# Optimization experiments

Measured on AMD Instinct MI355X. Metric: run time of the kernel, lower is better.

The kernel has to match this reference:

```python
import jax, jax.numpy as jnp
import numpy as np

EMBED_DIM = 1024
HEADS = 16
D_K = EMBED_DIM // HEADS
B, S = 2, 2048


def setup_inputs() -> dict:
    key = jax.random.key(0)
    ks = jax.random.split(key, 8)
    scale = 1.0 / np.sqrt(EMBED_DIM)
    inp = {
        "key": jax.random.normal(ks[0], (B, S, EMBED_DIM), dtype=jnp.float32),
        "query": jax.random.normal(ks[1], (B, S, EMBED_DIM), dtype=jnp.float32),
        "value": jax.random.normal(ks[2], (B, S, EMBED_DIM), dtype=jnp.float32),
        # torch nn.Linear stores weight as [out, in]; y = x @ W.T
        "Wq": jax.random.normal(ks[3], (EMBED_DIM, EMBED_DIM), dtype=jnp.float32) * scale,
        "Wk": jax.random.normal(ks[4], (EMBED_DIM, EMBED_DIM), dtype=jnp.float32) * scale,
        "Wv": jax.random.normal(ks[5], (EMBED_DIM, EMBED_DIM), dtype=jnp.float32) * scale,
        "Wo": jax.random.normal(ks[6], (EMBED_DIM, EMBED_DIM), dtype=jnp.float32) * scale,
        "bo": jax.random.normal(ks[7], (EMBED_DIM,), dtype=jnp.float32) * scale,
        # causal mask, True = keep (matches masked_fill(~mask, -1e20))
        "mask": jnp.tril(jnp.ones((S, S), dtype=jnp.bool_))[None, None, :, :],
    }
    return inp


def _split_heads(x):
    b, s, _ = x.shape
    return x.reshape(b, s, HEADS, D_K).transpose(0, 2, 1, 3)  # [B,H,S,d_k]


def reference(key, query, value, Wq, Wk, Wv, Wo, bo, mask):
    b, q_len = query.shape[0], query.shape[1]
    k = _split_heads(key @ Wk.T)
    q = _split_heads(query @ Wq.T)
    v = _split_heads(value @ Wv.T)
    scores = jnp.einsum('bhqd,bhkd->bhqk', q, k) / np.sqrt(D_K)
    scores = jnp.where(mask, scores, jnp.float32(-1e20))
    attn = jax.nn.softmax(scores, axis=-1)
    out = jnp.einsum('bhqk,bhkd->bhqd', attn, v)
    out = out.transpose(0, 2, 1, 3).reshape(b, q_len, HEADS * D_K)
    return out @ Wo.T + bo
```

## Files before the change

### kernel.cpp

```cpp
#include <hip/hip_runtime.h>
#include <cstdint>
#include <cstddef>


typedef __bf16 bf16;
typedef __bf16 bf16x4 __attribute__((ext_vector_type(4)));
typedef __bf16 bf16x8 __attribute__((ext_vector_type(8)));
typedef float f32x4 __attribute__((ext_vector_type(4)));

#define MFMA(a, b, c) __builtin_amdgcn_mfma_f32_16x16x32_bf16(a, b, c, 0, 0, 0)

constexpr int EMBED = 1024;
constexpr int SEQ = 2048;
constexpr int HEADS = 16;
constexpr int DK = 64;
constexpr int BH = 32;

__device__ __forceinline__ void gl16(const bf16* g, bf16* l) {
  __builtin_amdgcn_global_load_lds(
      (const __attribute__((address_space(1))) unsigned int*)g,
      (__attribute__((address_space(3))) unsigned int*)l, 16, 0, 0);
}

struct ConvArgs {
  const void* src[8];
  bf16* dst[8];
  int n8[8];
  const unsigned short* probe;
};

__global__ __launch_bounds__(256) void convert_kernel(ConvArgs a) {
  __shared__ int cnt;
  const int t = threadIdx.x;
  if (t == 0) cnt = 0;
  __syncthreads();
  {
    unsigned short u = a.probe[2 * t];
    int e = (u >> 7) & 0xFF;
    if (e >= 100 && e <= 130) atomicAdd(&cnt, 1);
  }
  __syncthreads();
  const int isf32 = (cnt < 128) ? 1 : 0;

  const int seg = blockIdx.y;
  const void* s = a.src[seg];
  bf16* d = a.dst[seg];
  const int n8 = a.n8[seg];
  for (int i = blockIdx.x * 256 + t; i < n8; i += gridDim.x * 256) {
    if (isf32) {
      const float* sp = (const float*)s + (size_t)i * 8;
      float4 x = *(const float4*)sp, y = *(const float4*)(sp + 4);
      bf16x8 v;
      v[0] = (bf16)x.x; v[1] = (bf16)x.y; v[2] = (bf16)x.z; v[3] = (bf16)x.w;
      v[4] = (bf16)y.x; v[5] = (bf16)y.y; v[6] = (bf16)y.z; v[7] = (bf16)y.w;
      *(bf16x8*)(d + (size_t)i * 8) = v;
    } else {
      *(uint4*)(d + (size_t)i * 8) = *(const uint4*)((const bf16*)s + (size_t)i * 8);
    }
  }
}

__device__ __forceinline__ void gemm_body(
    const bf16* __restrict__ X, const bf16* __restrict__ W,
    const bf16* __restrict__ bias, bf16* __restrict__ outb,
    float* __restrict__ outf, int mode, bf16* As, bf16* Bs, int m0, int n0)
{
  const int t = threadIdx.x;
  const int lane = t & 63, wave = t >> 6;
  const int wm = wave >> 2, wn = wave & 3;
  const int l16 = lane & 15, quad = lane >> 4;

  f32x4 acc[4][2] = {};

  for (int k0 = 0; k0 < EMBED; k0 += 64) {
    __syncthreads();
#pragma unroll
    for (int i = 0; i < 2; ++i) {
      int idx = t + i * 512;
      int r = idx >> 3;
      int cl = (idx & 7) ^ (r & 7);
      gl16(X + (size_t)(m0 + r) * EMBED + k0 + cl * 8, As + (i * 512 + wave * 64) * 8);
      gl16(W + (size_t)(n0 + r) * EMBED + k0 + cl * 8, Bs + (i * 512 + wave * 64) * 8);
    }
    __syncthreads();

#pragma unroll
    for (int ks = 0; ks < 2; ++ks) {
      bf16x8 a[4], b[2];
#pragma unroll
      for (int mi = 0; mi < 4; ++mi) {
        int row = wm * 64 + mi * 16 + l16;
        a[mi] = *(const bf16x8*)(As + row * 64 + (((ks * 4 + quad) ^ (row & 7)) * 8));
      }
#pragma unroll
      for (int ni = 0; ni < 2; ++ni) {
        int row = wn * 32 + ni * 16 + l16;
        b[ni] = *(const bf16x8*)(Bs + row * 64 + (((ks * 4 + quad) ^ (row & 7)) * 8));
      }
#pragma unroll
      for (int mi = 0; mi < 4; ++mi)
#pragma unroll
        for (int ni = 0; ni < 2; ++ni)
          acc[mi][ni] = MFMA(a[mi], b[ni], acc[mi][ni]);
    }
  }

#pragma unroll
  for (int mi = 0; mi < 4; ++mi) {
#pragma unroll
    for (int ni = 0; ni < 2; ++ni) {
      int n = n0 + wn * 32 + ni * 16 + l16;
#pragma unroll
      for (int r = 0; r < 4; ++r) {
        int m = m0 + wm * 64 + mi * 16 + quad * 4 + r;
        float v = acc[mi][ni][r];
        if (mode == 2) {
          outf[(size_t)m * EMBED + n] = v + (float)bias[n];
        } else {
          int b_ = m >> 11, s = m & (SEQ - 1);
          int h = n >> 6, d = n & 63;
          int bh = b_ * HEADS + h;
          if (mode == 0)
            outb[((size_t)bh * SEQ + s) * DK + d] = (bf16)v;
          else
            outb[((size_t)bh * DK + d) * SEQ + s] = (bf16)v;
        }
      }
    }
  }
}

struct QkvArgs {
  const bf16 *X0, *X1, *X2;
  const bf16 *W0, *W1, *W2;
  bf16 *O0, *O1, *O2;
};

__global__ __launch_bounds__(512, 4) void qkv_gemm(QkvArgs args) {
  __shared__ alignas(16) bf16 As[128 * 64];
  __shared__ alignas(16) bf16 Bs[128 * 64];
  const int z = blockIdx.z;
  const bf16* X = (z == 0) ? args.X0 : (z == 1) ? args.X1 : args.X2;
  const bf16* W = (z == 0) ? args.W0 : (z == 1) ? args.W1 : args.W2;
  bf16* O      = (z == 0) ? args.O0 : (z == 1) ? args.O1 : args.O2;
  int mode = (z == 2) ? 1 : 0;
  gemm_body(X, W, nullptr, O, nullptr, mode, As, Bs,
            blockIdx.x * 128, blockIdx.y * 128);
}

__global__ __launch_bounds__(512, 4) void out_gemm(const bf16* __restrict__ X,
                                                   const bf16* __restrict__ W,
                                                   const bf16* __restrict__ bias,
                                                   float* __restrict__ out) {
  __shared__ alignas(16) bf16 As[128 * 64];
  __shared__ alignas(16) bf16 Bs[128 * 64];
  gemm_body(X, W, bias, nullptr, out, 2, As, Bs,
            blockIdx.x * 128, blockIdx.y * 128);
}

__global__ __launch_bounds__(256, 6) void attn_kernel(
    const bf16* __restrict__ qbuf, const bf16* __restrict__ kbuf,
    const bf16* __restrict__ vtbuf, bf16* __restrict__ ctx)
{
  __shared__ alignas(16) bf16 Ks[64 * 64];
  __shared__ alignas(16) bf16 VTs[64 * 64];
  __shared__ alignas(16) bf16 Ps[64 * 72];

  const int t = threadIdx.x;
  const int g = (blockIdx.x + blockIdx.y) & 31;
  const int qt = (blockIdx.y & 16) ? (31 - g) : g;
  const int bh = blockIdx.y;
  const int q0 = qt * 64;
  const int lane = t & 63, w = t >> 6;
  const int l16 = lane & 15, quad = lane >> 4;

  const bf16* Kp0 = kbuf + (size_t)bh * SEQ * DK;
  const bf16* Vp0 = vtbuf + (size_t)bh * DK * SEQ;

  const bf16* Qg = qbuf + ((size_t)bh * SEQ + q0 + w * 16 + l16) * DK;
  bf16x8 qf[2];
  qf[0] = *(const bf16x8*)(Qg + quad * 8);
  qf[1] = *(const bf16x8*)(Qg + 32 + quad * 8);

  const int qglob = q0 + w * 16 + l16;
  float lst = 0.f;
  f32x4 o[4] = {};
  bf16* Pw = Ps + w * 16 * 72;

  constexpr float SC = 0.125f * 1.44269504f;
  constexpr float BI = -8.0f * 1.44269504f;

#pragma unroll 1
  for (int kt = 0; kt < qt; ++kt) {
    __syncthreads();
    const bf16* Kg = Kp0 + (size_t)kt * 64 * DK;
    const bf16* Vg = Vp0 + (size_t)kt * 64;
#pragma unroll
    for (int i = 0; i < 2; ++i) {
      int idx = t + i * 256;
      int r = idx >> 3;
      int cl = (idx & 7) ^ (r & 7);
      gl16(Kg + (size_t)r * DK + cl * 8, Ks + (i * 256 + w * 64) * 8);
      gl16(Vg + (size_t)r * SEQ + cl * 8, VTs + (i * 256 + w * 64) * 8);
    }
    __syncthreads();

    f32x4 sacc[4] = {};
#pragma unroll
    for (int ks = 0; ks < 2; ++ks) {
#pragma unroll
      for (int mi = 0; mi < 4; ++mi) {
        int row = mi * 16 + l16;
        bf16x8 kf = *(const bf16x8*)(Ks + row * 64 + (((ks * 4 + quad) ^ (row & 7)) * 8));
        sacc[mi] = MFMA(kf, qf[ks], sacc[mi]);
      }
    }

    float ls = 0.f;
#pragma unroll
    for (int mi = 0; mi < 4; ++mi) {
      bf16x4 pv;
#pragma unroll
      for (int r = 0; r < 4; ++r) {
        float p = __builtin_exp2f(__builtin_fmaf(sacc[mi][r], SC, BI));
        ls += p;
        pv[r] = (bf16)p;
      }
      *(bf16x4*)(Pw + l16 * 72 + mi * 16 + quad * 4) = pv;
    }
    ls += __shfl_xor(ls, 16);
    ls += __shfl_xor(ls, 32);
    lst += ls;

    __builtin_amdgcn_s_setprio(1);
#pragma unroll
    for (int ks = 0; ks < 2; ++ks) {
      bf16x8 pf = *(const bf16x8*)(Pw + l16 * 72 + ks * 32 + quad * 8);
#pragma unroll
      for (int dt = 0; dt < 4; ++dt) {
        int row = dt * 16 + l16;
        bf16x8 vf = *(const bf16x8*)(VTs + row * 64 +
                                     (((ks * 4 + quad) ^ (row & 7)) * 8));
        o[dt] = MFMA(vf, pf, o[dt]);
      }
    }
    __builtin_amdgcn_s_setprio(0);
  }

  {
    const int kt = qt;
    __syncthreads();
    const bf16* Kg = Kp0 + (size_t)kt * 64 * DK;
    const bf16* Vg = Vp0 + (size_t)kt * 64;
#pragma unroll
    for (int i = 0; i < 2; ++i) {
      int idx = t + i * 256;
      int r = idx >> 3;
      int cl = (idx & 7) ^ (r & 7);
      gl16(Kg + (size_t)r * DK + cl * 8, Ks + (i * 256 + w * 64) * 8);
      gl16(Vg + (size_t)r * SEQ + cl * 8, VTs + (i * 256 + w * 64) * 8);
    }
    __syncthreads();

    f32x4 sacc[4] = {};
#pragma unroll
    for (int ks = 0; ks < 2; ++ks) {
#pragma unroll
      for (int mi = 0; mi < 4; ++mi) {
        int row = mi * 16 + l16;
        bf16x8 kf = *(const bf16x8*)(Ks + row * 64 + (((ks * 4 + quad) ^ (row & 7)) * 8));
        sacc[mi] = MFMA(kf, qf[ks], sacc[mi]);
      }
    }

    float ls = 0.f;
    const int kbase = kt * 64 + quad * 4;
#pragma unroll
    for (int mi = 0; mi < 4; ++mi) {
      bf16x4 pv;
#pragma unroll
      for (int r = 0; r < 4; ++r) {
        float arg = __builtin_fmaf(sacc[mi][r], SC, BI);
        if (kbase + mi * 16 + r > qglob) arg = -1e30f;
        float p = __builtin_exp2f(arg);
        ls += p;
        pv[r] = (bf16)p;
      }
      *(bf16x4*)(Pw + l16 * 72 + mi * 16 + quad * 4) = pv;
    }
    ls += __shfl_xor(ls, 16);
    ls += __shfl_xor(ls, 32);
    lst += ls;

    __builtin_amdgcn_s_setprio(1);
#pragma unroll
    for (int ks = 0; ks < 2; ++ks) {
      bf16x8 pf = *(const bf16x8*)(Pw + l16 * 72 + ks * 32 + quad * 8);
#pragma unroll
      for (int dt = 0; dt < 4; ++dt) {
        int row = dt * 16 + l16;
        bf16x8 vf = *(const bf16x8*)(VTs + row * 64 +
                                     (((ks * 4 + quad) ^ (row & 7)) * 8));
        o[dt] = MFMA(vf, pf, o[dt]);
      }
    }
    __builtin_amdgcn_s_setprio(0);
  }

  const float inv = 1.0f / lst;
  const int b_ = bh >> 4, h = bh & 15;
  bf16* dst = ctx + ((size_t)b_ * SEQ + qglob) * EMBED + h * DK;
#pragma unroll
  for (int dt = 0; dt < 4; ++dt) {
    bf16x4 v;
#pragma unroll
    for (int r = 0; r < 4; ++r) v[r] = (bf16)(o[dt][r] * inv);
    *(bf16x4*)(dst + dt * 16 + quad * 4) = v;
  }
}

extern "C" void kernel_launch(void* const* d_in, const int* in_sizes, int n_in,
                              void* d_out, int out_size, void* d_ws, size_t ws_size,
                              hipStream_t stream) {
  const void* key   = d_in[0];
  const void* query = d_in[1];
  const void* value = d_in[2];
  const void* Wq    = d_in[3];
  const void* Wk    = d_in[4];
  const void* Wv    = d_in[5];
  const void* Wo    = d_in[6];
  const void* bo    = d_in[7];
  float* out = (float*)d_out;

  char* base = (char*)d_ws + 256;
  const size_t XN = (size_t)2 * SEQ * EMBED;
  const size_t WN = (size_t)EMBED * EMBED;
  const size_t per = (size_t)BH * SEQ * DK;

  bf16* cq  = (bf16*)base;
  bf16* ck  = cq + XN;
  bf16* cv  = ck + XN;
  bf16* cWq = cv + XN;
  bf16* cWk = cWq + WN;
  bf16* cWv = cWk + WN;
  bf16* cWo = cWv + WN;
  bf16* cbo = cWo + WN;
  bf16* qb  = cbo + 1024;
  bf16* kb  = qb + per;
  bf16* vtb = kb + per;
  bf16* ctx = vtb + per;

  ConvArgs ca;
  ca.src[0] = query; ca.dst[0] = cq;  ca.n8[0] = (int)(XN / 8);
  ca.src[1] = key;   ca.dst[1] = ck;  ca.n8[1] = (int)(XN / 8);
  ca.src[2] = value; ca.dst[2] = cv;  ca.n8[2] = (int)(XN / 8);
  ca.src[3] = Wq;    ca.dst[3] = cWq; ca.n8[3] = (int)(WN / 8);
  ca.src[4] = Wk;    ca.dst[4] = cWk; ca.n8[4] = (int)(WN / 8);
  ca.src[5] = Wv;    ca.dst[5] = cWv; ca.n8[5] = (int)(WN / 8);
  ca.src[6] = Wo;    ca.dst[6] = cWo; ca.n8[6] = (int)(WN / 8);
  ca.src[7] = bo;    ca.dst[7] = cbo; ca.n8[7] = 128;
  ca.probe = (const unsigned short*)Wq;
  convert_kernel<<<dim3(512, 8), 256, 0, stream>>>(ca);

  QkvArgs qa{cq, ck, cv, cWq, cWk, cWv, qb, kb, vtb};
  qkv_gemm<<<dim3(32, 8, 3), 512, 0, stream>>>(qa);
  attn_kernel<<<dim3(32, 32), 256, 0, stream>>>(qb, kb, vtb, ctx);
  out_gemm<<<dim3(32, 8), 512, 0, stream>>>(ctx, cWo, cbo, out);
}
```

Baseline: 229.0 us.

## Split attention key tiles across two wave halves with LDS reduction

The attention kernel now launches 512 threads per block instead of 256. Two groups of four waves each handle one 32-key half of every 64-key tile for the same 16 query rows. Their partial output accumulators and row sums are combined through shared memory at the end. This doubles the waves per block, which should add latency hiding and cut the serial per-wave work in long causal rows. The cost is an extra cross-wave reduction and more waves sharing the same barriers.

```diff
diff --git a/kernel.cpp b/kernel.cpp
--- a/kernel.cpp
+++ b/kernel.cpp
@@ -158,13 +158,77 @@
             blockIdx.x * 128, blockIdx.y * 128);
 }
 
-__global__ __launch_bounds__(256, 6) void attn_kernel(
+template<bool MASKED>
+__device__ __forceinline__ void attn_step(
+    int kt, int t, int w, int half, int l16, int quad, int qglob,
+    const bf16* __restrict__ Kp0, const bf16* __restrict__ Vp0,
+    bf16* Ks, bf16* VTs, bf16* Pw,
+    const bf16x8 qf[2], f32x4 o[4], float& lst)
+{
+  constexpr float SC = 0.125f * 1.44269504f;
+  constexpr float BI = -8.0f * 1.44269504f;
+
+  __syncthreads();
+  {
+    int r = t >> 3;
+    int cl = (t & 7) ^ (r & 7);
+    gl16(Kp0 + ((size_t)kt * 64 + r) * DK + cl * 8, Ks + w * 512);
+    gl16(Vp0 + (size_t)r * SEQ + kt * 64 + cl * 8, VTs + w * 512);
+  }
+  __syncthreads();
+
+  f32x4 sacc[2] = {};
+#pragma unroll
+  for (int ks = 0; ks < 2; ++ks) {
+#pragma unroll
+    for (int mi = 0; mi < 2; ++mi) {
+      int row = half * 32 + mi * 16 + l16;
+      bf16x8 kf = *(const bf16x8*)(Ks + row * 64 + (((ks * 4 + quad) ^ (row & 7)) * 8));
+      sacc[mi] = MFMA(kf, qf[ks], sacc[mi]);
+    }
+  }
+
+  float ls = 0.f;
+#pragma unroll
+  for (int mi = 0; mi < 2; ++mi) {
+    bf16x4 pv;
+#pragma unroll
+    for (int r = 0; r < 4; ++r) {
+      float arg = __builtin_fmaf(sacc[mi][r], SC, BI);
+      if (MASKED) {
+        int kg = kt * 64 + half * 32 + mi * 16 + quad * 4 + r;
+        if (kg > qglob) arg = -1e30f;
+      }
+      float p = __builtin_exp2f(arg);
+      ls += p;
+      pv[r] = (bf16)p;
+    }
+    *(bf16x4*)(Pw + l16 * 36 + mi * 16 + quad * 4) = pv;
+  }
+  ls += __shfl_xor(ls, 16);
+  ls += __shfl_xor(ls, 32);
+  lst += ls;
+
+  __builtin_amdgcn_s_setprio(1);
+  bf16x8 pf = *(const bf16x8*)(Pw + l16 * 36 + quad * 8);
+#pragma unroll
+  for (int dt = 0; dt < 4; ++dt) {
+    int row = dt * 16 + l16;
+    bf16x8 vf = *(const bf16x8*)(VTs + row * 64 +
+                                 (((half * 4 + quad) ^ (row & 7)) * 8));
+    o[dt] = MFMA(vf, pf, o[dt]);
+  }
+  __builtin_amdgcn_s_setprio(0);
+}
+
+__global__ __launch_bounds__(512, 8) void attn_kernel(
     const bf16* __restrict__ qbuf, const bf16* __restrict__ kbuf,
     const bf16* __restrict__ vtbuf, bf16* __restrict__ ctx)
 {
-  __shared__ alignas(16) bf16 Ks[64 * 64];
-  __shared__ alignas(16) bf16 VTs[64 * 64];
-  __shared__ alignas(16) bf16 Ps[64 * 72];
+  __shared__ alignas(16) unsigned char SM[25600];
+  bf16* Ks  = (bf16*)SM;
+  bf16* VTs = (bf16*)(SM + 8192);
+  bf16* Ps  = (bf16*)(SM + 16384);
 
   const int t = threadIdx.x;
   const int g = (blockIdx.x + blockIdx.y) & 31;
@@ -172,150 +236,53 @@
   const int bh = blockIdx.y;
   const int q0 = qt * 64;
   const int lane = t & 63, w = t >> 6;
+  const int wq = w & 3, half = w >> 2;
   const int l16 = lane & 15, quad = lane >> 4;
 
   const bf16* Kp0 = kbuf + (size_t)bh * SEQ * DK;
   const bf16* Vp0 = vtbuf + (size_t)bh * DK * SEQ;
 
-  const bf16* Qg = qbuf + ((size_t)bh * SEQ + q0 + w * 16 + l16) * DK;
+  const bf16* Qg = qbuf + ((size_t)bh * SEQ + q0 + wq * 16 + l16) * DK;
   bf16x8 qf[2];
   qf[0] = *(const bf16x8*)(Qg + quad * 8);
   qf[1] = *(const bf16x8*)(Qg + 32 + quad * 8);
 
-  const int qglob = q0 + w * 16 + l16;
+  const int qglob = q0 + wq * 16 + l16;
   float lst = 0.f;
   f32x4 o[4] = {};
-  bf16* Pw = Ps + w * 16 * 72;
-
-  constexpr float SC = 0.125f * 1.44269504f;
-  constexpr float BI = -8.0f * 1.44269504f;
+  bf16* Pw = Ps + w * (16 * 36);
 
 #pragma unroll 1
-  for (int kt = 0; kt < qt; ++kt) {
-    __syncthreads();
-    const bf16* Kg = Kp0 + (size_t)kt * 64 * DK;
-    const bf16* Vg = Vp0 + (size_t)kt * 64;
-#pragma unroll
-    for (int i = 0; i < 2; ++i) {
-      int idx = t + i * 256;
-      int r = idx >> 3;
-      int cl = (idx & 7) ^ (r & 7);
-      gl16(Kg + (size_t)r * DK + cl * 8, Ks + (i * 256 + w * 64) * 8);
-      gl16(Vg + (size_t)r * SEQ + cl * 8, VTs + (i * 256 + w * 64) * 8);
-    }
-    __syncthreads();
-
-    f32x4 sacc[4] = {};
-#pragma unroll
-    for (int ks = 0; ks < 2; ++ks) {
-#pragma unroll
-      for (int mi = 0; mi < 4; ++mi) {
-        int row = mi * 16 + l16;
-        bf16x8 kf = *(const bf16x8*)(Ks + row * 64 + (((ks * 4 + quad) ^ (row & 7)) * 8));
-        sacc[mi] = MFMA(kf, qf[ks], sacc[mi]);
-      }
-    }
-
-    float ls = 0.f;
-#pragma unroll
-    for (int mi = 0; mi < 4; ++mi) {
-      bf16x4 pv;
-#pragma unroll
-      for (int r = 0; r < 4; ++r) {
-        float p = __builtin_exp2f(__builtin_fmaf(sacc[mi][r], SC, BI));
-        ls += p;
-        pv[r] = (bf16)p;
-      }
-      *(bf16x4*)(Pw + l16 * 72 + mi * 16 + quad * 4) = pv;
-    }
-    ls += __shfl_xor(ls, 16);
-    ls += __shfl_xor(ls, 32);
-    lst += ls;
-
-    __builtin_amdgcn_s_setprio(1);
-#pragma unroll
-    for (int ks = 0; ks < 2; ++ks) {
-      bf16x8 pf = *(const bf16x8*)(Pw + l16 * 72 + ks * 32 + quad * 8);
-#pragma unroll
-      for (int dt = 0; dt < 4; ++dt) {
-        int row = dt * 16 + l16;
-        bf16x8 vf = *(const bf16x8*)(VTs + row * 64 +
-                                     (((ks * 4 + quad) ^ (row & 7)) * 8));
-        o[dt] = MFMA(vf, pf, o[dt]);
-      }
-    }
-    __builtin_amdgcn_s_setprio(0);
-  }
-
-  {
-    const int kt = qt;
-    __syncthreads();
-    const bf16* Kg = Kp0 + (size_t)kt * 64 * DK;
-    const bf16* Vg = Vp0 + (size_t)kt * 64;
-#pragma unroll
-    for (int i = 0; i < 2; ++i) {
-      int idx = t + i * 256;
-      int r = idx >> 3;
-      int cl = (idx & 7) ^ (r & 7);
-      gl16(Kg + (size_t)r * DK + cl * 8, Ks + (i * 256 + w * 64) * 8);
-      gl16(Vg + (size_t)r * SEQ + cl * 8, VTs + (i * 256 + w * 64) * 8);
-    }
-    __syncthreads();
-
-    f32x4 sacc[4] = {};
-#pragma unroll
-    for (int ks = 0; ks < 2; ++ks) {
-#pragma unroll
-      for (int mi = 0; mi < 4; ++mi) {
-        int row = mi * 16 + l16;
-        bf16x8 kf = *(const bf16x8*)(Ks + row * 64 + (((ks * 4 + quad) ^ (row & 7)) * 8));
-        sacc[mi] = MFMA(kf, qf[ks], sacc[mi]);
-      }
-    }
-
-    float ls = 0.f;
-    const int kbase = kt * 64 + quad * 4;
-#pragma unroll
-    for (int mi = 0; mi < 4; ++mi) {
-      bf16x4 pv;
-#pragma unroll
-      for (int r = 0; r < 4; ++r) {
-        float arg = __builtin_fmaf(sacc[mi][r], SC, BI);
-        if (kbase + mi * 16 + r > qglob) arg = -1e30f;
-        float p = __builtin_exp2f(arg);
-        ls += p;
-        pv[r] = (bf16)p;
-      }
-      *(bf16x4*)(Pw + l16 * 72 + mi * 16 + quad * 4) = pv;
-    }
-    ls += __shfl_xor(ls, 16);
-    ls += __shfl_xor(ls, 32);
-    lst += ls;
-
-    __builtin_amdgcn_s_setprio(1);
-#pragma unroll
-    for (int ks = 0; ks < 2; ++ks) {
-      bf16x8 pf = *(const bf16x8*)(Pw + l16 * 72 + ks * 32 + quad * 8);
-#pragma unroll
-      for (int dt = 0; dt < 4; ++dt) {
-        int row = dt * 16 + l16;
-        bf16x8 vf = *(const bf16x8*)(VTs + row * 64 +
-                                     (((ks * 4 + quad) ^ (row & 7)) * 8));
-        o[dt] = MFMA(vf, pf, o[dt]);
-      }
-    }
-    __builtin_amdgcn_s_setprio(0);
-  }
-
-  const float inv = 1.0f / lst;
-  const int b_ = bh >> 4, h = bh & 15;
-  bf16* dst = ctx + ((size_t)b_ * SEQ + qglob) * EMBED + h * DK;
-#pragma unroll
-  for (int dt = 0; dt < 4; ++dt) {
-    bf16x4 v;
-#pragma unroll
-    for (int r = 0; r < 4; ++r) v[r] = (bf16)(o[dt][r] * inv);
-    *(bf16x4*)(dst + dt * 16 + quad * 4) = v;
+  for (int kt = 0; kt < qt; ++kt)
+    attn_step<false>(kt, t, w, half, l16, quad, qglob, Kp0, Vp0, Ks, VTs, Pw, qf, o, lst);
+  attn_step<true>(qt, t, w, half, l16, quad, qglob, Kp0, Vp0, Ks, VTs, Pw, qf, o, lst);
+
+  __syncthreads();
+  float* Co = (float*)SM;
+  float* Cl = (float*)(SM + 16384);
+  if (half) {
+    int base = ((w - 4) * 64 + lane) * 16;
+#pragma unroll
+    for (int dt = 0; dt < 4; ++dt) *(f32x4*)(Co + base + dt * 4) = o[dt];
+    Cl[(w - 4) * 64 + lane] = lst;
+  }
+  __syncthreads();
+  if (!half) {
+    int base = (w * 64 + lane) * 16;
+#pragma unroll
+    for (int dt = 0; dt < 4; ++dt) o[dt] += *(const f32x4*)(Co + base + dt * 4);
+    lst += Cl[w * 64 + lane];
+
+    const float inv = 1.0f / lst;
+    const int b_ = bh >> 4, h = bh & 15;
+    bf16* dst = ctx + ((size_t)b_ * SEQ + qglob) * EMBED + h * DK;
+#pragma unroll
+    for (int dt = 0; dt < 4; ++dt) {
+      bf16x4 v;
+#pragma unroll
+      for (int r = 0; r < 4; ++r) v[r] = (bf16)(o[dt][r] * inv);
+      *(bf16x4*)(dst + dt * 16 + quad * 4) = v;
+    }
   }
 }
 
@@ -364,6 +331,6 @@
 
   QkvArgs qa{cq, ck, cv, cWq, cWk, cWv, qb, kb, vtb};
   qkv_gemm<<<dim3(32, 8, 3), 512, 0, stream>>>(qa);
-  attn_kernel<<<dim3(32, 32), 256, 0, stream>>>(qb, kb, vtb, ctx);
+  attn_kernel<<<dim3(32, 32), 512, 0, stream>>>(qb, kb, vtb, ctx);
   out_gemm<<<dim3(32, 8), 512, 0, stream>>>(ctx, cWo, cbo, out);
 }
```

New measurement: 247.5 us. +8.1%, slower.

## Split long causal attention rows across two blocks with a combine kernel

Applied to the files above, without the earlier changes.

Causal attention for query tiles 16-31 is split into two blocks, one covering KV tiles 0-15 and one covering the rest. Each writes unnormalized fp32 partial outputs and row sums to workspace, and a new combine kernel merges them into ctx. The aim is to even out per-block work and cut the tail caused by the longest query tiles. The cost is an extra kernel launch, fp32 partial traffic, and a workspace-size check that falls back to the monolithic kernel when space is short. The combine is valid because a fixed exponent bias is used instead of a running max.

```diff
diff --git a/kernel.cpp b/kernel.cpp
--- a/kernel.cpp
+++ b/kernel.cpp
@@ -158,7 +158,166 @@
             blockIdx.x * 128, blockIdx.y * 128);
 }
 
-__global__ __launch_bounds__(256, 6) void attn_kernel(
+template<bool MASKED>
+__device__ __forceinline__ void attn_tile(
+    int kt, int t, int w, int l16, int quad, int qglob,
+    const bf16* __restrict__ Kp0, const bf16* __restrict__ Vp0,
+    bf16* Ks, bf16* VTs, bf16* Pw,
+    const bf16x8 qf[2], f32x4 o[4], float& lst)
+{
+  constexpr float SC = 0.125f * 1.44269504f;
+  constexpr float BI = -8.0f * 1.44269504f;
+
+  __syncthreads();
+  const bf16* Kg = Kp0 + (size_t)kt * 64 * DK;
+  const bf16* Vg = Vp0 + (size_t)kt * 64;
+#pragma unroll
+  for (int i = 0; i < 2; ++i) {
+    int idx = t + i * 256;
+    int r = idx >> 3;
+    int cl = (idx & 7) ^ (r & 7);
+    gl16(Kg + (size_t)r * DK + cl * 8, Ks + (i * 256 + w * 64) * 8);
+    gl16(Vg + (size_t)r * SEQ + cl * 8, VTs + (i * 256 + w * 64) * 8);
+  }
+  __syncthreads();
+
+  f32x4 sacc[4] = {};
+#pragma unroll
+  for (int ks = 0; ks < 2; ++ks) {
+#pragma unroll
+    for (int mi = 0; mi < 4; ++mi) {
+      int row = mi * 16 + l16;
+      bf16x8 kf = *(const bf16x8*)(Ks + row * 64 + (((ks * 4 + quad) ^ (row & 7)) * 8));
+      sacc[mi] = MFMA(kf, qf[ks], sacc[mi]);
+    }
+  }
+
+  float ls = 0.f;
+  const int kbase = kt * 64 + quad * 4;
+#pragma unroll
+  for (int mi = 0; mi < 4; ++mi) {
+    bf16x4 pv;
+#pragma unroll
+    for (int r = 0; r < 4; ++r) {
+      float arg = __builtin_fmaf(sacc[mi][r], SC, BI);
+      if (MASKED && (kbase + mi * 16 + r > qglob)) arg = -1e30f;
+      float p = __builtin_exp2f(arg);
+      ls += p;
+      pv[r] = (bf16)p;
+    }
+    *(bf16x4*)(Pw + l16 * 72 + mi * 16 + quad * 4) = pv;
+  }
+  ls += __shfl_xor(ls, 16);
+  ls += __shfl_xor(ls, 32);
+  lst += ls;
+
+  __builtin_amdgcn_s_setprio(1);
+#pragma unroll
+  for (int ks = 0; ks < 2; ++ks) {
+    bf16x8 pf = *(const bf16x8*)(Pw + l16 * 72 + ks * 32 + quad * 8);
+#pragma unroll
+    for (int dt = 0; dt < 4; ++dt) {
+      int row = dt * 16 + l16;
+      bf16x8 vf = *(const bf16x8*)(VTs + row * 64 +
+                                   (((ks * 4 + quad) ^ (row & 7)) * 8));
+      o[dt] = MFMA(vf, pf, o[dt]);
+    }
+  }
+  __builtin_amdgcn_s_setprio(0);
+}
+
+__global__ __launch_bounds__(256, 6) void attn_split(
+    const bf16* __restrict__ qbuf, const bf16* __restrict__ kbuf,
+    const bf16* __restrict__ vtbuf, bf16* __restrict__ ctx,
+    float* __restrict__ po, float* __restrict__ pl)
+{
+  __shared__ alignas(16) bf16 Ks[64 * 64];
+  __shared__ alignas(16) bf16 VTs[64 * 64];
+  __shared__ alignas(16) bf16 Ps[64 * 72];
+
+  const int t = threadIdx.x;
+  const int s = blockIdx.x;
+  const int bh = blockIdx.y;
+  const int mode = (s < 16) ? 0 : (s < 32) ? 1 : 2;
+  const int qt = (mode == 2) ? (s - 16) : s;
+  const int t0 = (mode == 2) ? 16 : 0;
+  const int t1 = (mode == 1) ? 15 : qt;
+  const int q0 = qt * 64;
+  const int lane = t & 63, w = t >> 6;
+  const int l16 = lane & 15, quad = lane >> 4;
+
+  const bf16* Kp0 = kbuf + (size_t)bh * SEQ * DK;
+  const bf16* Vp0 = vtbuf + (size_t)bh * DK * SEQ;
+
+  const bf16* Qg = qbuf + ((size_t)bh * SEQ + q0 + w * 16 + l16) * DK;
+  bf16x8 qf[2];
+  qf[0] = *(const bf16x8*)(Qg + quad * 8);
+  qf[1] = *(const bf16x8*)(Qg + 32 + quad * 8);
+
+  const int qglob = q0 + w * 16 + l16;
+  float lst = 0.f;
+  f32x4 o[4] = {};
+  bf16* Pw = Ps + w * 16 * 72;
+
+  const int tEnd = (mode == 1) ? t1 : t1 - 1;
+#pragma unroll 1
+  for (int kt = t0; kt <= tEnd; ++kt)
+    attn_tile<false>(kt, t, w, l16, quad, qglob, Kp0, Vp0, Ks, VTs, Pw, qf, o, lst);
+  if (mode != 1)
+    attn_tile<true>(t1, t, w, l16, quad, qglob, Kp0, Vp0, Ks, VTs, Pw, qf, o, lst);
+
+  if (mode == 0) {
+    const float inv = 1.0f / lst;
+    const int b_ = bh >> 4, h = bh & 15;
+    bf16* dst = ctx + ((size_t)b_ * SEQ + qglob) * EMBED + h * DK;
+#pragma unroll
+    for (int dt = 0; dt < 4; ++dt) {
+      bf16x4 v;
+#pragma unroll
+      for (int r = 0; r < 4; ++r) v[r] = (bf16)(o[dt][r] * inv);
+      *(bf16x4*)(dst + dt * 16 + quad * 4) = v;
+    }
+  } else {
+    const int p = ((bh << 4) + (qt - 16)) * 2 + (mode - 1);
+    float* ob = po + (size_t)p * 4096;
+    const int qloc = w * 16 + l16;
+#pragma unroll
+    for (int dt = 0; dt < 4; ++dt)
+      *(f32x4*)(ob + qloc * 64 + dt * 16 + quad * 4) = o[dt];
+    if (quad == 0) pl[(size_t)p * 64 + qloc] = lst;
+  }
+}
+
+__global__ __launch_bounds__(256) void attn_combine(
+    const float* __restrict__ po, const float* __restrict__ pl,
+    bf16* __restrict__ ctx)
+{
+  const int p0 = blockIdx.x;
+  const int bh = p0 >> 4, qtl = p0 & 15, qt = 16 + qtl;
+  const int t = threadIdx.x;
+  const float* o0 = po + (size_t)p0 * 2 * 4096;
+  const float* o1 = o0 + 4096;
+  const float* l0 = pl + (size_t)p0 * 2 * 64;
+  const float* l1 = l0 + 64;
+
+  const int q = t >> 2;
+  const int d0 = (t & 3) * 16;
+  const float inv = 1.0f / (l0[q] + l1[q]);
+
+  const int b_ = bh >> 4, h = bh & 15;
+  bf16* dst = ctx + ((size_t)b_ * SEQ + qt * 64 + q) * EMBED + h * DK + d0;
+#pragma unroll
+  for (int j = 0; j < 4; ++j) {
+    f32x4 a = *(const f32x4*)(o0 + q * 64 + d0 + j * 4);
+    f32x4 b = *(const f32x4*)(o1 + q * 64 + d0 + j * 4);
+    bf16x4 v;
+#pragma unroll
+    for (int r = 0; r < 4; ++r) v[r] = (bf16)((a[r] + b[r]) * inv);
+    *(bf16x4*)(dst + j * 4) = v;
+  }
+}
+
+__global__ __launch_bounds__(256, 6) void attn_mono(
     const bf16* __restrict__ qbuf, const bf16* __restrict__ kbuf,
     const bf16* __restrict__ vtbuf, bf16* __restrict__ ctx)
 {
@@ -187,125 +346,10 @@
   f32x4 o[4] = {};
   bf16* Pw = Ps + w * 16 * 72;
 
-  constexpr float SC = 0.125f * 1.44269504f;
-  constexpr float BI = -8.0f * 1.44269504f;
-
 #pragma unroll 1
-  for (int kt = 0; kt < qt; ++kt) {
-    __syncthreads();
-    const bf16* Kg = Kp0 + (size_t)kt * 64 * DK;
-    const bf16* Vg = Vp0 + (size_t)kt * 64;
-#pragma unroll
-    for (int i = 0; i < 2; ++i) {
-      int idx = t + i * 256;
-      int r = idx >> 3;
-      int cl = (idx & 7) ^ (r & 7);
-      gl16(Kg + (size_t)r * DK + cl * 8, Ks + (i * 256 + w * 64) * 8);
-      gl16(Vg + (size_t)r * SEQ + cl * 8, VTs + (i * 256 + w * 64) * 8);
-    }
-    __syncthreads();
-
-    f32x4 sacc[4] = {};
-#pragma unroll
-    for (int ks = 0; ks < 2; ++ks) {
-#pragma unroll
-      for (int mi = 0; mi < 4; ++mi) {
-        int row = mi * 16 + l16;
-        bf16x8 kf = *(const bf16x8*)(Ks + row * 64 + (((ks * 4 + quad) ^ (row & 7)) * 8));
-        sacc[mi] = MFMA(kf, qf[ks], sacc[mi]);
-      }
-    }
-
-    float ls = 0.f;
-#pragma unroll
-    for (int mi = 0; mi < 4; ++mi) {
-      bf16x4 pv;
-#pragma unroll
-      for (int r = 0; r < 4; ++r) {
-        float p = __builtin_exp2f(__builtin_fmaf(sacc[mi][r], SC, BI));
-        ls += p;
-        pv[r] = (bf16)p;
-      }
-      *(bf16x4*)(Pw + l16 * 72 + mi * 16 + quad * 4) = pv;
-    }
-    ls += __shfl_xor(ls, 16);
-    ls += __shfl_xor(ls, 32);
-    lst += ls;
-
-    __builtin_amdgcn_s_setprio(1);
-#pragma unroll
-    for (int ks = 0; ks < 2; ++ks) {
-      bf16x8 pf = *(const bf16x8*)(Pw + l16 * 72 + ks * 32 + quad * 8);
-#pragma unroll
-      for (int dt = 0; dt < 4; ++dt) {
-        int row = dt * 16 + l16;
-        bf16x8 vf = *(const bf16x8*)(VTs + row * 64 +
-                                     (((ks * 4 + quad) ^ (row & 7)) * 8));
-        o[dt] = MFMA(vf, pf, o[dt]);
-      }
-    }
-    __builtin_amdgcn_s_setprio(0);
-  }
-
-  {
-    const int kt = qt;
-    __syncthreads();
-    const bf16* Kg = Kp0 + (size_t)kt * 64 * DK;
-    const bf16* Vg = Vp0 + (size_t)kt * 64;
-#pragma unroll
-    for (int i = 0; i < 2; ++i) {
-      int idx = t + i * 256;
-      int r = idx >> 3;
-      int cl = (idx & 7) ^ (r & 7);
-      gl16(Kg + (size_t)r * DK + cl * 8, Ks + (i * 256 + w * 64) * 8);
-      gl16(Vg + (size_t)r * SEQ + cl * 8, VTs + (i * 256 + w * 64) * 8);
-    }
-    __syncthreads();
-
-    f32x4 sacc[4] = {};
-#pragma unroll
-    for (int ks = 0; ks < 2; ++ks) {
-#pragma unroll
-      for (int mi = 0; mi < 4; ++mi) {
-        int row = mi * 16 + l16;
-        bf16x8 kf = *(const bf16x8*)(Ks + row * 64 + (((ks * 4 + quad) ^ (row & 7)) * 8));
-        sacc[mi] = MFMA(kf, qf[ks], sacc[mi]);
-      }
-    }
-
-    float ls = 0.f;
-    const int kbase = kt * 64 + quad * 4;
-#pragma unroll
-    for (int mi = 0; mi < 4; ++mi) {
-      bf16x4 pv;
-#pragma unroll
-      for (int r = 0; r < 4; ++r) {
-        float arg = __builtin_fmaf(sacc[mi][r], SC, BI);
-        if (kbase + mi * 16 + r > qglob) arg = -1e30f;
-        float p = __builtin_exp2f(arg);
-        ls += p;
-        pv[r] = (bf16)p;
-      }
-      *(bf16x4*)(Pw + l16 * 72 + mi * 16 + quad * 4) = pv;
-    }
-    ls += __shfl_xor(ls, 16);
-    ls += __shfl_xor(ls, 32);
-    lst += ls;
-
-    __builtin_amdgcn_s_setprio(1);
-#pragma unroll
-    for (int ks = 0; ks < 2; ++ks) {
-      bf16x8 pf = *(const bf16x8*)(Pw + l16 * 72 + ks * 32 + quad * 8);
-#pragma unroll
-      for (int dt = 0; dt < 4; ++dt) {
-        int row = dt * 16 + l16;
-        bf16x8 vf = *(const bf16x8*)(VTs + row * 64 +
-                                     (((ks * 4 + quad) ^ (row & 7)) * 8));
-        o[dt] = MFMA(vf, pf, o[dt]);
-      }
-    }
-    __builtin_amdgcn_s_setprio(0);
-  }
+  for (int kt = 0; kt < qt; ++kt)
+    attn_tile<false>(kt, t, w, l16, quad, qglob, Kp0, Vp0, Ks, VTs, Pw, qf, o, lst);
+  attn_tile<true>(qt, t, w, l16, quad, qglob, Kp0, Vp0, Ks, VTs, Pw, qf, o, lst);
 
   const float inv = 1.0f / lst;
   const int b_ = bh >> 4, h = bh & 15;
@@ -350,6 +394,12 @@
   bf16* vtb = kb + per;
   bf16* ctx = vtb + per;
 
+  float* po = (float*)(ctx + per);
+  float* pl = po + (size_t)512 * 2 * 4096;
+  const size_t need = 256 + (3 * XN + 4 * WN + 1024 + 4 * per) * sizeof(bf16)
+                    + (size_t)512 * 2 * 4096 * 4 + (size_t)512 * 2 * 64 * 4;
+  const bool split_ok = (ws_size >= need);
+
   ConvArgs ca;
   ca.src[0] = query; ca.dst[0] = cq;  ca.n8[0] = (int)(XN / 8);
   ca.src[1] = key;   ca.dst[1] = ck;  ca.n8[1] = (int)(XN / 8);
@@ -364,6 +414,13 @@
 
   QkvArgs qa{cq, ck, cv, cWq, cWk, cWv, qb, kb, vtb};
   qkv_gemm<<<dim3(32, 8, 3), 512, 0, stream>>>(qa);
-  attn_kernel<<<dim3(32, 32), 256, 0, stream>>>(qb, kb, vtb, ctx);
+
+  if (split_ok) {
+    attn_split<<<dim3(48, 32), 256, 0, stream>>>(qb, kb, vtb, ctx, po, pl);
+    attn_combine<<<dim3(512), 256, 0, stream>>>(po, pl, ctx);
+  } else {
+    attn_mono<<<dim3(32, 32), 256, 0, stream>>>(qb, kb, vtb, ctx);
+  }
+
   out_gemm<<<dim3(32, 8), 512, 0, stream>>>(ctx, cWo, cbo, out);
 }
```

New measurement: 228.4 us. Within noise of the previous version (-0.3%).

## Split long causal attention rows across two blocks and add a combine kernel

Applied to the files above, without the earlier changes.

Attention now uses 128-row query tiles in which each wave handles 32 query rows, so every loaded K/V tile feeds twice as many MFMAs. For the second half of the sequence the key range is split between two blocks, which write unnormalized fp32 partial outputs and row sums to workspace, and a small combine kernel merges them. Blocks are mapped to XCDs by head. The aim is to balance the triangular causal workload and improve K/V reuse. The cost is an extra kernel launch, fp32 partial traffic, and lower occupancy. The old path is kept as a fallback when the workspace is too small.

```diff
diff --git a/kernel.cpp b/kernel.cpp
--- a/kernel.cpp
+++ b/kernel.cpp
@@ -158,7 +158,256 @@
             blockIdx.x * 128, blockIdx.y * 128);
 }
 
-__global__ __launch_bounds__(256, 6) void attn_kernel(
+template<bool MASKED>
+__device__ __forceinline__ void attn_tile2(
+    int kt, int t, int w, int l16, int quad, int qbase,
+    const bf16* __restrict__ Kp0, const bf16* __restrict__ Vp0,
+    bf16* Ks, bf16* VTs, bf16* Pw,
+    const bf16x8 qf[2][2], f32x4 o[2][4], float lst[2])
+{
+  constexpr float SC = 0.125f * 1.44269504f;
+  constexpr float BI = -8.0f * 1.44269504f;
+
+  __syncthreads();
+  const bf16* Kg = Kp0 + (size_t)kt * 64 * DK;
+  const bf16* Vg = Vp0 + (size_t)kt * 64;
+#pragma unroll
+  for (int i = 0; i < 2; ++i) {
+    int idx = t + i * 256;
+    int r = idx >> 3;
+    int cl = (idx & 7) ^ (r & 7);
+    gl16(Kg + (size_t)r * DK + cl * 8, Ks + (i * 256 + w * 64) * 8);
+    gl16(Vg + (size_t)r * SEQ + cl * 8, VTs + (i * 256 + w * 64) * 8);
+  }
+  __syncthreads();
+
+  f32x4 sacc[2][4] = {};
+#pragma unroll
+  for (int ks = 0; ks < 2; ++ks) {
+#pragma unroll
+    for (int mi = 0; mi < 4; ++mi) {
+      int row = mi * 16 + l16;
+      bf16x8 kf = *(const bf16x8*)(Ks + row * 64 + (((ks * 4 + quad) ^ (row & 7)) * 8));
+      sacc[0][mi] = MFMA(kf, qf[0][ks], sacc[0][mi]);
+      sacc[1][mi] = MFMA(kf, qf[1][ks], sacc[1][mi]);
+    }
+  }
+
+#pragma unroll
+  for (int g = 0; g < 2; ++g) {
+    const int qg = qbase + g * 16 + l16;
+    float ls = 0.f;
+#pragma unroll
+    for (int mi = 0; mi < 4; ++mi) {
+      bf16x4 pv;
+#pragma unroll
+      for (int r = 0; r < 4; ++r) {
+        float arg = __builtin_fmaf(sacc[g][mi][r], SC, BI);
+        if (MASKED && (kt * 64 + mi * 16 + quad * 4 + r > qg)) arg = -1e30f;
+        float p = __builtin_exp2f(arg);
+        ls += p;
+        pv[r] = (bf16)p;
+      }
+      *(bf16x4*)(Pw + (g * 16 + l16) * 72 + mi * 16 + quad * 4) = pv;
+    }
+    ls += __shfl_xor(ls, 16);
+    ls += __shfl_xor(ls, 32);
+    lst[g] += ls;
+  }
+
+  __builtin_amdgcn_s_setprio(1);
+#pragma unroll
+  for (int ks = 0; ks < 2; ++ks) {
+    bf16x8 pf0 = *(const bf16x8*)(Pw + l16 * 72 + ks * 32 + quad * 8);
+    bf16x8 pf1 = *(const bf16x8*)(Pw + (16 + l16) * 72 + ks * 32 + quad * 8);
+#pragma unroll
+    for (int dt = 0; dt < 4; ++dt) {
+      int row = dt * 16 + l16;
+      bf16x8 vf = *(const bf16x8*)(VTs + row * 64 +
+                                   (((ks * 4 + quad) ^ (row & 7)) * 8));
+      o[0][dt] = MFMA(vf, pf0, o[0][dt]);
+      o[1][dt] = MFMA(vf, pf1, o[1][dt]);
+    }
+  }
+  __builtin_amdgcn_s_setprio(0);
+}
+
+__global__ __launch_bounds__(256, 3) void attn_split(
+    const bf16* __restrict__ qbuf, const bf16* __restrict__ kbuf,
+    const bf16* __restrict__ vtbuf, bf16* __restrict__ ctx,
+    float* __restrict__ po, float* __restrict__ pl)
+{
+  __shared__ alignas(16) bf16 Ks[64 * 64];
+  __shared__ alignas(16) bf16 VTs[64 * 64];
+  __shared__ alignas(16) bf16 Ps[4 * 32 * 72];
+
+  const int t = threadIdx.x;
+  const int gid = blockIdx.x;
+  const int xcd = gid & 7, j = gid >> 3;
+  const int bh = xcd + ((j & 3) << 3);
+  const int s = j >> 2;
+  const int mode = (s < 8) ? 0 : (s < 16) ? 1 : 2;
+  const int qt = (mode == 2) ? (s - 8) : s;
+  const int q0 = qt * 128;
+  const int lane = t & 63, w = t >> 6;
+  const int l16 = lane & 15, quad = lane >> 4;
+  const int qbase = q0 + w * 32;
+
+  const bf16* Kp0 = kbuf + (size_t)bh * SEQ * DK;
+  const bf16* Vp0 = vtbuf + (size_t)bh * DK * SEQ;
+
+  bf16x8 qf[2][2];
+#pragma unroll
+  for (int g = 0; g < 2; ++g) {
+    const bf16* Qg = qbuf + ((size_t)bh * SEQ + qbase + g * 16 + l16) * DK;
+    qf[g][0] = *(const bf16x8*)(Qg + quad * 8);
+    qf[g][1] = *(const bf16x8*)(Qg + 32 + quad * 8);
+  }
+
+  float lst[2] = {0.f, 0.f};
+  f32x4 o[2][4] = {};
+  bf16* Pw = Ps + w * (32 * 72);
+
+  const int t0 = (mode == 2) ? 16 : 0;
+  const int tEnd = (mode == 1) ? 15 : (2 * qt - 1);
+#pragma unroll 1
+  for (int kt = t0; kt <= tEnd; ++kt)
+    attn_tile2<false>(kt, t, w, l16, quad, qbase, Kp0, Vp0, Ks, VTs, Pw, qf, o, lst);
+  if (mode != 1) {
+    attn_tile2<true>(2 * qt, t, w, l16, quad, qbase, Kp0, Vp0, Ks, VTs, Pw, qf, o, lst);
+    attn_tile2<true>(2 * qt + 1, t, w, l16, quad, qbase, Kp0, Vp0, Ks, VTs, Pw, qf, o, lst);
+  }
+
+  if (mode == 0) {
+    const int b_ = bh >> 4, h = bh & 15;
+#pragma unroll
+    for (int g = 0; g < 2; ++g) {
+      const float inv = 1.0f / lst[g];
+      bf16* dst = ctx + ((size_t)b_ * SEQ + qbase + g * 16 + l16) * EMBED + h * DK;
+#pragma unroll
+      for (int dt = 0; dt < 4; ++dt) {
+        bf16x4 v;
+#pragma unroll
+        for (int r = 0; r < 4; ++r) v[r] = (bf16)(o[g][dt][r] * inv);
+        *(bf16x4*)(dst + dt * 16 + quad * 4) = v;
+      }
+    }
+  } else {
+    const int p = ((bh << 3) + (qt - 8)) * 2 + (mode - 1);
+    float* ob = po + (size_t)p * 8192;
+#pragma unroll
+    for (int g = 0; g < 2; ++g) {
+      const int qloc = w * 32 + g * 16 + l16;
+#pragma unroll
+      for (int dt = 0; dt < 4; ++dt)
+        *(f32x4*)(ob + qloc * 64 + dt * 16 + quad * 4) = o[g][dt];
+      if (quad == 0) pl[(size_t)p * 128 + qloc] = lst[g];
+    }
+  }
+}
+
+__global__ __launch_bounds__(256) void attn_combine(
+    const float* __restrict__ po, const float* __restrict__ pl,
+    bf16* __restrict__ ctx)
+{
+  const int gid = blockIdx.x;
+  const int xcd = gid & 7, j = gid >> 3;
+  const int bh = xcd + ((j & 3) << 3);
+  const int qtl = j >> 2;
+  const int p0 = (bh << 3) + qtl;
+  const int qt = 8 + qtl;
+  const int t = threadIdx.x;
+  const float* o0 = po + (size_t)p0 * 2 * 8192;
+  const float* o1 = o0 + 8192;
+  const float* l0 = pl + (size_t)p0 * 2 * 128;
+  const float* l1 = l0 + 128;
+
+  const int q = t >> 1;
+  const int d0 = (t & 1) * 32;
+  const float inv = 1.0f / (l0[q] + l1[q]);
+
+  const int b_ = bh >> 4, h = bh & 15;
+  bf16* dst = ctx + ((size_t)b_ * SEQ + qt * 128 + q) * EMBED + h * DK + d0;
+#pragma unroll
+  for (int jj = 0; jj < 8; ++jj) {
+    f32x4 a = *(const f32x4*)(o0 + q * 64 + d0 + jj * 4);
+    f32x4 b = *(const f32x4*)(o1 + q * 64 + d0 + jj * 4);
+    bf16x4 v;
+#pragma unroll
+    for (int r = 0; r < 4; ++r) v[r] = (bf16)((a[r] + b[r]) * inv);
+    *(bf16x4*)(dst + jj * 4) = v;
+  }
+}
+
+template<bool MASKED>
+__device__ __forceinline__ void attn_tile(
+    int kt, int t, int w, int l16, int quad, int qglob,
+    const bf16* __restrict__ Kp0, const bf16* __restrict__ Vp0,
+    bf16* Ks, bf16* VTs, bf16* Pw,
+    const bf16x8 qf[2], f32x4 o[4], float& lst)
+{
+  constexpr float SC = 0.125f * 1.44269504f;
+  constexpr float BI = -8.0f * 1.44269504f;
+
+  __syncthreads();
+  const bf16* Kg = Kp0 + (size_t)kt * 64 * DK;
+  const bf16* Vg = Vp0 + (size_t)kt * 64;
+#pragma unroll
+  for (int i = 0; i < 2; ++i) {
+    int idx = t + i * 256;
+    int r = idx >> 3;
+    int cl = (idx & 7) ^ (r & 7);
+    gl16(Kg + (size_t)r * DK + cl * 8, Ks + (i * 256 + w * 64) * 8);
+    gl16(Vg + (size_t)r * SEQ + cl * 8, VTs + (i * 256 + w * 64) * 8);
+  }
+  __syncthreads();
+
+  f32x4 sacc[4] = {};
+#pragma unroll
+  for (int ks = 0; ks < 2; ++ks) {
+#pragma unroll
+    for (int mi = 0; mi < 4; ++mi) {
+      int row = mi * 16 + l16;
+      bf16x8 kf = *(const bf16x8*)(Ks + row * 64 + (((ks * 4 + quad) ^ (row & 7)) * 8));
+      sacc[mi] = MFMA(kf, qf[ks], sacc[mi]);
+    }
+  }
+
+  float ls = 0.f;
+  const int kbase = kt * 64 + quad * 4;
+#pragma unroll
+  for (int mi = 0; mi < 4; ++mi) {
+    bf16x4 pv;
+#pragma unroll
+    for (int r = 0; r < 4; ++r) {
+      float arg = __builtin_fmaf(sacc[mi][r], SC, BI);
+      if (MASKED && (kbase + mi * 16 + r > qglob)) arg = -1e30f;
+      float p = __builtin_exp2f(arg);
+      ls += p;
+      pv[r] = (bf16)p;
+    }
+    *(bf16x4*)(Pw + l16 * 72 + mi * 16 + quad * 4) = pv;
+  }
+  ls += __shfl_xor(ls, 16);
+  ls += __shfl_xor(ls, 32);
+  lst += ls;
+
+  __builtin_amdgcn_s_setprio(1);
+#pragma unroll
+  for (int ks = 0; ks < 2; ++ks) {
+    bf16x8 pf = *(const bf16x8*)(Pw + l16 * 72 + ks * 32 + quad * 8);
+#pragma unroll
+    for (int dt = 0; dt < 4; ++dt) {
+      int row = dt * 16 + l16;
+      bf16x8 vf = *(const bf16x8*)(VTs + row * 64 +
+                                   (((ks * 4 + quad) ^ (row & 7)) * 8));
+      o[dt] = MFMA(vf, pf, o[dt]);
+    }
+  }
+  __builtin_amdgcn_s_setprio(0);
+}
+
+__global__ __launch_bounds__(256, 6) void attn_mono(
     const bf16* __restrict__ qbuf, const bf16* __restrict__ kbuf,
     const bf16* __restrict__ vtbuf, bf16* __restrict__ ctx)
 {
@@ -187,125 +436,10 @@
   f32x4 o[4] = {};
   bf16* Pw = Ps + w * 16 * 72;
 
-  constexpr float SC = 0.125f * 1.44269504f;
-  constexpr float BI = -8.0f * 1.44269504f;
-
 #pragma unroll 1
-  for (int kt = 0; kt < qt; ++kt) {
-    __syncthreads();
-    const bf16* Kg = Kp0 + (size_t)kt * 64 * DK;
-    const bf16* Vg = Vp0 + (size_t)kt * 64;
-#pragma unroll
-    for (int i = 0; i < 2; ++i) {
-      int idx = t + i * 256;
-      int r = idx >> 3;
-      int cl = (idx & 7) ^ (r & 7);
-      gl16(Kg + (size_t)r * DK + cl * 8, Ks + (i * 256 + w * 64) * 8);
-      gl16(Vg + (size_t)r * SEQ + cl * 8, VTs + (i * 256 + w * 64) * 8);
-    }
-    __syncthreads();
-
-    f32x4 sacc[4] = {};
-#pragma unroll
-    for (int ks = 0; ks < 2; ++ks) {
-#pragma unroll
-      for (int mi = 0; mi < 4; ++mi) {
-        int row = mi * 16 + l16;
-        bf16x8 kf = *(const bf16x8*)(Ks + row * 64 + (((ks * 4 + quad) ^ (row & 7)) * 8));
-        sacc[mi] = MFMA(kf, qf[ks], sacc[mi]);
-      }
-    }
-
-    float ls = 0.f;
-#pragma unroll
-    for (int mi = 0; mi < 4; ++mi) {
-      bf16x4 pv;
-#pragma unroll
-      for (int r = 0; r < 4; ++r) {
-        float p = __builtin_exp2f(__builtin_fmaf(sacc[mi][r], SC, BI));
-        ls += p;
-        pv[r] = (bf16)p;
-      }
-      *(bf16x4*)(Pw + l16 * 72 + mi * 16 + quad * 4) = pv;
-    }
-    ls += __shfl_xor(ls, 16);
-    ls += __shfl_xor(ls, 32);
-    lst += ls;
-
-    __builtin_amdgcn_s_setprio(1);
-#pragma unroll
-    for (int ks = 0; ks < 2; ++ks) {
-      bf16x8 pf = *(const bf16x8*)(Pw + l16 * 72 + ks * 32 + quad * 8);
-#pragma unroll
-      for (int dt = 0; dt < 4; ++dt) {
-        int row = dt * 16 + l16;
-        bf16x8 vf = *(const bf16x8*)(VTs + row * 64 +
-                                     (((ks * 4 + quad) ^ (row & 7)) * 8));
-        o[dt] = MFMA(vf, pf, o[dt]);
-      }
-    }
-    __builtin_amdgcn_s_setprio(0);
-  }
-
-  {
-    const int kt = qt;
-    __syncthreads();
-    const bf16* Kg = Kp0 + (size_t)kt * 64 * DK;
-    const bf16* Vg = Vp0 + (size_t)kt * 64;
-#pragma unroll
-    for (int i = 0; i < 2; ++i) {
-      int idx = t + i * 256;
-      int r = idx >> 3;
-      int cl = (idx & 7) ^ (r & 7);
-      gl16(Kg + (size_t)r * DK + cl * 8, Ks + (i * 256 + w * 64) * 8);
-      gl16(Vg + (size_t)r * SEQ + cl * 8, VTs + (i * 256 + w * 64) * 8);
-    }
-    __syncthreads();
-
-    f32x4 sacc[4] = {};
-#pragma unroll
-    for (int ks = 0; ks < 2; ++ks) {
-#pragma unroll
-      for (int mi = 0; mi < 4; ++mi) {
-        int row = mi * 16 + l16;
-        bf16x8 kf = *(const bf16x8*)(Ks + row * 64 + (((ks * 4 + quad) ^ (row & 7)) * 8));
-        sacc[mi] = MFMA(kf, qf[ks], sacc[mi]);
-      }
-    }
-
-    float ls = 0.f;
-    const int kbase = kt * 64 + quad * 4;
-#pragma unroll
-    for (int mi = 0; mi < 4; ++mi) {
-      bf16x4 pv;
-#pragma unroll
-      for (int r = 0; r < 4; ++r) {
-        float arg = __builtin_fmaf(sacc[mi][r], SC, BI);
-        if (kbase + mi * 16 + r > qglob) arg = -1e30f;
-        float p = __builtin_exp2f(arg);
-        ls += p;
-        pv[r] = (bf16)p;
-      }
-      *(bf16x4*)(Pw + l16 * 72 + mi * 16 + quad * 4) = pv;
-    }
-    ls += __shfl_xor(ls, 16);
-    ls += __shfl_xor(ls, 32);
-    lst += ls;
-
-    __builtin_amdgcn_s_setprio(1);
-#pragma unroll
-    for (int ks = 0; ks < 2; ++ks) {
-      bf16x8 pf = *(const bf16x8*)(Pw + l16 * 72 + ks * 32 + quad * 8);
-#pragma unroll
-      for (int dt = 0; dt < 4; ++dt) {
-        int row = dt * 16 + l16;
-        bf16x8 vf = *(const bf16x8*)(VTs + row * 64 +
-                                     (((ks * 4 + quad) ^ (row & 7)) * 8));
-        o[dt] = MFMA(vf, pf, o[dt]);
-      }
-    }
-    __builtin_amdgcn_s_setprio(0);
-  }
+  for (int kt = 0; kt < qt; ++kt)
+    attn_tile<false>(kt, t, w, l16, quad, qglob, Kp0, Vp0, Ks, VTs, Pw, qf, o, lst);
+  attn_tile<true>(qt, t, w, l16, quad, qglob, Kp0, Vp0, Ks, VTs, Pw, qf, o, lst);
 
   const float inv = 1.0f / lst;
   const int b_ = bh >> 4, h = bh & 15;
@@ -350,6 +484,12 @@
   bf16* vtb = kb + per;
   bf16* ctx = vtb + per;
 
+  float* po = (float*)(ctx + per);
+  float* pl = po + (size_t)256 * 2 * 8192;
+  const size_t need = 256 + (3 * XN + 4 * WN + 1024 + 4 * per) * sizeof(bf16)
+                    + (size_t)256 * 2 * 8192 * 4 + (size_t)256 * 2 * 128 * 4;
+  const bool split_ok = (ws_size >= need);
+
   ConvArgs ca;
   ca.src[0] = query; ca.dst[0] = cq;  ca.n8[0] = (int)(XN / 8);
   ca.src[1] = key;   ca.dst[1] = ck;  ca.n8[1] = (int)(XN / 8);
@@ -364,6 +504,13 @@
 
   QkvArgs qa{cq, ck, cv, cWq, cWk, cWv, qb, kb, vtb};
   qkv_gemm<<<dim3(32, 8, 3), 512, 0, stream>>>(qa);
-  attn_kernel<<<dim3(32, 32), 256, 0, stream>>>(qb, kb, vtb, ctx);
+
+  if (split_ok) {
+    attn_split<<<dim3(768), 256, 0, stream>>>(qb, kb, vtb, ctx, po, pl);
+    attn_combine<<<dim3(256), 256, 0, stream>>>(po, pl, ctx);
+  } else {
+    attn_mono<<<dim3(32, 32), 256, 0, stream>>>(qb, kb, vtb, ctx);
+  }
+
   out_gemm<<<dim3(32, 8), 512, 0, stream>>>(ctx, cWo, cbo, out);
 }
```

New measurement: 245.7 us. 1.07x slower.
